# Optimization experiments

Measured on AMD Instinct MI355X. Metric: run time of the kernel, lower is better.

Reference implementation:

```python
import jax, jax.numpy as jnp
import numpy as np

B, N, DIM, IN_DIM, H = 8, 3136, 147, 64, 1
HD = IN_DIM // H          # per-head value/key dim = 64
MLP_HID = int(IN_DIM * 1.0)
EPS = 1e-5


def _ln(x, w, b):
    m = jnp.mean(x, axis=-1, keepdims=True)
    v = jnp.mean((x - m) ** 2, axis=-1, keepdims=True)
    return (x - m) / jnp.sqrt(v + EPS) * w + b


def setup_inputs() -> dict:
    key = jax.random.key(0)
    ks = jax.random.split(key, 12)
    r = lambda k, shp, s=0.02: (jax.random.normal(k, shp, dtype=jnp.float32) * s)
    return {
        "x": jax.random.normal(ks[0], (B, N, DIM), dtype=jnp.float32),
        "norm1_w": jnp.ones((DIM,), jnp.float32),
        "norm1_b": jnp.zeros((DIM,), jnp.float32),
        "qkv_w": r(ks[1], (3 * IN_DIM, DIM)),
        "scale": jnp.full((H,), (DIM // H) ** -0.5, dtype=jnp.float32),
        "proj_w": r(ks[2], (IN_DIM, IN_DIM)),
        "proj_b": jnp.zeros((IN_DIM,), jnp.float32),
        "norm2_w": jnp.ones((IN_DIM,), jnp.float32),
        "norm2_b": jnp.zeros((IN_DIM,), jnp.float32),
        "fc1_w": r(ks[3], (MLP_HID, IN_DIM)),
        "fc1_b": jnp.zeros((MLP_HID,), jnp.float32),
        "fc2_w": r(ks[4], (IN_DIM, MLP_HID)),
        "fc2_b": jnp.zeros((IN_DIM,), jnp.float32),
    }


def reference(x, norm1_w, norm1_b, qkv_w, scale, proj_w, proj_b,
              norm2_w, norm2_b, fc1_w, fc1_b, fc2_w, fc2_b):
    h = _ln(x, norm1_w, norm1_b)                               # [B,N,DIM]
    qkv = jnp.einsum('bnc,oc->bno', h, qkv_w)                  # [B,N,3*IN_DIM]
    qkv = qkv.reshape(B, N, 3, H, HD).transpose(2, 0, 3, 1, 4)  # [3,B,H,N,HD]
    q, k, v = qkv[0], qkv[1], qkv[2]
    # LMSA: learnable per-head scale + diagonal (self) exclusion mask
    attn = jnp.einsum('bhid,bhjd->bhij', q, k) * scale[None, :, None, None]
    eye = jnp.eye(N, dtype=bool)
    attn = jnp.where(eye[None, None], -jnp.inf, attn)
    attn = jax.nn.softmax(attn, axis=-1)
    o = jnp.einsum('bhij,bhjd->bhid', attn, v)                 # [B,H,N,HD]
    o = o.transpose(0, 2, 1, 3).reshape(B, N, IN_DIM)
    o = jnp.einsum('bnd,od->bno', o, proj_w) + proj_b
    # num_heads == 1 -> residual is v itself
    x_attn = v[:, 0] + o                                       # [B,N,IN_DIM]
    h2 = _ln(x_attn, norm2_w, norm2_b)
    h2 = jax.nn.gelu(jnp.einsum('bnd,hd->bnh', h2, fc1_w) + fc1_b,
                     approximate=False)
    h2 = jnp.einsum('bnh,oh->bno', h2, fc2_w) + fc2_b
    return x_attn + h2
```

## Files before the change

### kernel.cpp

```cpp
#include <hip/hip_runtime.h>
#include <math.h>
#include <stdint.h>

#define B_    8
#define N_    3136
#define DIM_  147
#define KP_   160
#define TOK_  (B_*N_)
#define QKV3_ 192
#define NSPLIT 4

typedef __attribute__((ext_vector_type(4)))  float f32x4;
typedef __attribute__((ext_vector_type(16))) float f32x16;
typedef __attribute__((ext_vector_type(4)))  unsigned int u32x4;
typedef __attribute__((ext_vector_type(2)))  unsigned int u32x2;
typedef __attribute__((ext_vector_type(8)))  short short8;
typedef float f32x4u __attribute__((ext_vector_type(4), aligned(4)));
typedef union { short8 s; u32x4 u; } pk8;

static __device__ __forceinline__ unsigned short f2b(float f){
  unsigned int u = __float_as_uint(f);
  u += 0x7fffu + ((u>>16)&1u);
  return (unsigned short)(u>>16);
}
static __device__ __forceinline__ unsigned int pk2(float a, float b){
  return ((unsigned int)f2b(b)<<16) | (unsigned int)f2b(a);
}
static __device__ __forceinline__ unsigned int pk2t(float a, float b){
  return (__float_as_uint(b) & 0xffff0000u) | (__float_as_uint(a)>>16);
}
static __device__ __forceinline__ float b2f(unsigned short s){
  return __uint_as_float(((unsigned int)s)<<16);
}

#define GLD16(gp, lp) __builtin_amdgcn_global_load_lds( \
    reinterpret_cast<const uint32_t __attribute__((address_space(1)))*>(reinterpret_cast<uintptr_t>(gp)), \
    reinterpret_cast<uint32_t __attribute__((address_space(3)))*>(reinterpret_cast<uintptr_t>(lp)), \
    16, 0, 0)

__global__ __launch_bounds__(256) void k_qkv(const float* __restrict__ x,
                                             const float* __restrict__ w1,
                                             const float* __restrict__ b1,
                                             const float* __restrict__ qkvw,
                                             const float* __restrict__ scale,
                                             unsigned short* __restrict__ qb,
                                             unsigned short* __restrict__ kb,
                                             unsigned short* __restrict__ vtb,
                                             unsigned short* __restrict__ vfb){
  __shared__ alignas(16) unsigned short Wb[192*168];
  unsigned short* A_ = Wb;
  unsigned short* VT = Wb;
  int tid = threadIdx.x;
  int w = tid>>6, lane = tid&63, quad = lane>>4, l16 = lane&15;
  int t0 = blockIdx.x*64;
  float sc2 = scale[0] * 1.44269504089f;

  #pragma unroll
  for(int half=0; half<2; half++){
    int g = half*32 + (tid>>3), e = tid&7;
    const float* xr = x + (size_t)(t0+g)*147;
    f32x4u xv[5];
    float s = 0.f, sq = 0.f;
    #pragma unroll
    for(int j=0;j<5;j++){
      int k = e + 8*j;
      int keff = (k > 36) ? 36 : k;
      f32x4u v = *(const f32x4u*)(xr + 4*keff);
      if(j == 4){
        v[0] = (k<=36) ? v[0] : 0.f;
        v[1] = (k<=36) ? v[1] : 0.f;
        v[2] = (k<=36) ? v[2] : 0.f;
        v[3] = (k< 36) ? v[3] : 0.f;
      }
      xv[j] = v;
      s  += (v[0]+v[1]) + (v[2]+v[3]);
      sq += (v[0]*v[0]+v[1]*v[1]) + (v[2]*v[2]+v[3]*v[3]);
    }
    s  += __shfl_xor(s,1,64);  s  += __shfl_xor(s,2,64);  s  += __shfl_xor(s,4,64);
    sq += __shfl_xor(sq,1,64); sq += __shfl_xor(sq,2,64); sq += __shfl_xor(sq,4,64);
    float mean = s*(1.f/147.f);
    float var  = sq*(1.f/147.f) - mean*mean;
    float rstd = rsqrtf(var + 1e-5f);
    #pragma unroll
    for(int j=0;j<5;j++){
      int k = e + 8*j;
      unsigned int lo = 0u, hi = 0u;
      if(k <= 36){
        int c0 = 4*k;
        int c3 = (k==36) ? 146 : c0+3;
        float y0 = (xv[j][0]-mean)*rstd*w1[c0]   + b1[c0];
        float y1 = (xv[j][1]-mean)*rstd*w1[c0+1] + b1[c0+1];
        float y2 = (xv[j][2]-mean)*rstd*w1[c0+2] + b1[c0+2];
        float y3 = (xv[j][3]-mean)*rstd*w1[c3]   + b1[c3];
        if(k == 36) y3 = 0.f;
        lo = pk2(y0,y1); hi = pk2(y2,y3);
      }
      *(u32x2*)(A_ + g*168 + 4*k) = (u32x2){lo,hi};
    }
  }
  __syncthreads();
  short8 Af[5];
  #pragma unroll
  for(int kk=0;kk<5;kk++)
    Af[kk] = *(const short8*)(A_ + (w*16+l16)*168 + kk*32 + quad*8);
  __syncthreads();
  {
    unsigned int* dst = (unsigned int*)Wb;
    #pragma unroll
    for(int rep=0; rep<15; rep++){
      int idx = rep*256 + tid;
      int row = idx/20, c = idx - row*20;
      u32x4 o = (u32x4){0u,0u,0u,0u};
      if(c < 19){
        const float* sp = qkvw + row*147 + c*8;
        f32x4u a = *(const f32x4u*)sp;
        o[0] = pk2(a[0],a[1]);
        if(c < 18){
          f32x4u bv = *(const f32x4u*)(sp+4);
          o[1] = pk2(a[2],a[3]);
          o[2] = pk2(bv[0],bv[1]);
          o[3] = pk2(bv[2],bv[3]);
        } else {
          o[1] = pk2(a[2],0.f);
        }
      }
      *(u32x4*)(dst + row*84 + c*4) = o;
    }
  }
  __syncthreads();
  f32x4 acc[12];
  #pragma unroll
  for(int i=0;i<12;i++) acc[i] = (f32x4){0.f,0.f,0.f,0.f};
  #pragma unroll
  for(int nt=0;nt<12;nt++){
    #pragma unroll
    for(int kk=0;kk<5;kk++){
      short8 Bf = *(const short8*)(Wb + (nt*16+l16)*168 + kk*32 + quad*8);
      acc[nt] = __builtin_amdgcn_mfma_f32_16x16x32_bf16(Af[kk], Bf, acc[nt], 0,0,0);
    }
  }
  #pragma unroll
  for(int nt=0;nt<12;nt++){
    int o = nt*16 + l16;
    #pragma unroll
    for(int r=0;r<4;r++){
      int tl = w*16 + quad*4 + r;
      int mg = t0 + tl;
      float val = acc[nt][r];
      if(o < 64)        qb[(size_t)mg*64 + o]        = f2b(val*sc2);
      else if(o < 128)  kb[(size_t)mg*64 + (o-64)]   = f2b(val);
      else              vfb[(size_t)mg*64 + (o-128)] = f2b(val);
    }
  }
  __syncthreads();
  #pragma unroll
  for(int nt=8;nt<12;nt++){
    int hd = (nt-8)*16 + l16;
    #pragma unroll
    for(int r=0;r<4;r++)
      VT[hd*72 + (w*16 + quad*4 + r)] = f2b(acc[nt][r]);
  }
  __syncthreads();
  {
    int b = t0 / N_, n0 = t0 - b*N_;
    const unsigned int* VT32 = (const unsigned int*)VT;
    unsigned int* vg = (unsigned int*)vtb + ((size_t)b*64)*(N_/2) + (n0>>1);
    #pragma unroll
    for(int rep=0;rep<8;rep++){
      int f = rep*256 + tid;
      int row = f>>5, c = f&31;
      vg[(size_t)row*(N_/2) + c] = VT32[row*36 + c];
    }
  }
}

__global__ __launch_bounds__(128,2) void k_attn(const unsigned short* __restrict__ qb,
                                                const unsigned short* __restrict__ kb,
                                                const unsigned short* __restrict__ vtb,
                                                unsigned short* __restrict__ Opart,
                                                float* __restrict__ lpart){
  __shared__ alignas(16) unsigned int L[8192];
  __shared__ float Lr[128];
  int tid = threadIdx.x;
  int w = tid>>6, lane = tid&63;
  int h = lane>>5, l32 = lane&31, l7 = l32&7;
  int qt = blockIdx.x, sp = blockIdx.y, b = blockIdx.z;
  int q0 = qt*64;
  int kv0 = (sp*49)>>2, kv1 = ((sp+1)*49)>>2;
  int nt = kv1 - kv0;

  short8 Qf[2][4];
  {
    const unsigned short* qg = qb + ((size_t)b*N_ + q0)*64;
    #pragma unroll
    for(int qh=0;qh<2;qh++)
      #pragma unroll
      for(int kc=0;kc<4;kc++)
        Qf[qh][kc] = *(const short8*)(qg + (32*qh + l32)*64 + 16*kc + 8*h);
  }
  int koffG[4], voffG[4];
  {
    int pl = lane>>3, cl = lane&7;
    #pragma unroll
    for(int rr=0;rr<4;rr++){
      int p = rr*8 + pl;
      int sig = (p & 0x13) | ((p&4)<<1) | ((p&8)>>1);
      int cx = cl ^ (p&7);
      koffG[rr] = (32*w + sig)*128 + cx*16;
      voffG[rr] = (32*w + p)*(N_*2) + cx*16;
    }
  }
  const char* kBase = (const char*)kb + (size_t)b*N_*128;
  const char* vBase = (const char*)vtb + (size_t)b*64*(size_t)(N_*2);

  f32x16 O[2][2];
  #pragma unroll
  for(int qh=0;qh<2;qh++) for(int hdq=0;hdq<2;hdq++)
    #pragma unroll
    for(int r=0;r<16;r++) O[qh][hdq][r] = 0.f;
  float lracc[2][4];
  #pragma unroll
  for(int qh=0;qh<2;qh++)
    #pragma unroll
    for(int j=0;j<4;j++) lracc[qh][j] = 0.f;

  {
    const char* kT = kBase + (size_t)kv0*8192;
    const char* vT = vBase + (size_t)kv0*128;
    #pragma unroll
    for(int rr=0;rr<4;rr++) GLD16(kT + koffG[rr], (char*)L + w*4096 + rr*1024);
    #pragma unroll
    for(int rr=0;rr<4;rr++) GLD16(vT + voffG[rr], (char*)L + 8192 + w*4096 + rr*1024);
  }

  int cur = 0;
  for(int i=0;i<nt;i++){
    int kvt = kv0 + i;
    if(i+1 < nt){
      const char* kT = kBase + (size_t)(kvt+1)*8192;
      const char* vT = vBase + (size_t)(kvt+1)*128;
      char* dst = (char*)L + (cur^1)*16384;
      #pragma unroll
      for(int rr=0;rr<4;rr++) GLD16(kT + koffG[rr], dst + w*4096 + rr*1024);
      #pragma unroll
      for(int rr=0;rr<4;rr++) GLD16(vT + voffG[rr], dst + 8192 + w*4096 + rr*1024);
      asm volatile("s_waitcnt vmcnt(8)" ::: "memory");
    } else {
      asm volatile("s_waitcnt vmcnt(0)" ::: "memory");
    }
    __builtin_amdgcn_s_barrier();
    __builtin_amdgcn_sched_barrier(0);

    const unsigned short* Kh = (const unsigned short*)L + cur*8192 + w*2048;
    const unsigned short* Vh = (const unsigned short*)L + cur*8192 + 4096;

    short8 Kf[4];
    #pragma unroll
    for(int kc=0;kc<4;kc++)
      Kf[kc] = *(const short8*)(Kh + l32*64 + (((2*kc+h) ^ l7)&7)*8);
    #pragma unroll
    for(int qh=0;qh<2;qh++){
      f32x16 S;
      #pragma unroll
      for(int r=0;r<16;r++) S[r] = 0.f;
      #pragma unroll
      for(int kc=0;kc<4;kc++)
        S = __builtin_amdgcn_mfma_f32_32x32x16_bf16(Kf[kc], Qf[qh][kc], S, 0,0,0);
      f32x16 E;
      if(kvt == qt){
        int dref = 32*qh + l32 - 32*w - 8*h;
        #pragma unroll
        for(int r=0;r<16;r++){
          int kvl = 16*((r>>3)&1) + 4*((r>>2)&1) + (r&3);
          float pv = (kvl == dref) ? 0.f : __builtin_amdgcn_exp2f(S[r]);
          E[r] = pv; lracc[qh][r&3] += pv;
        }
      } else {
        #pragma unroll
        for(int r=0;r<16;r++){
          float pv = __builtin_amdgcn_exp2f(S[r]);
          E[r] = pv; lracc[qh][r&3] += pv;
        }
      }
      pk8 Pb0, Pb1;
      Pb0.u = (u32x4){ pk2t(E[0],E[1]),   pk2t(E[2],E[3]),
                       pk2t(E[4],E[5]),   pk2t(E[6],E[7]) };
      Pb1.u = (u32x4){ pk2t(E[8],E[9]),   pk2t(E[10],E[11]),
                       pk2t(E[12],E[13]), pk2t(E[14],E[15]) };
      #pragma unroll
      for(int hdq=0;hdq<2;hdq++){
        short8 Vf0 = *(const short8*)(Vh + (32*hdq + l32)*64 + (((4*w + h) ^ l7)&7)*8);
        short8 Vf1 = *(const short8*)(Vh + (32*hdq + l32)*64 + (((4*w + 2 + h) ^ l7)&7)*8);
        O[qh][hdq] = __builtin_amdgcn_mfma_f32_32x32x16_bf16(Vf0, Pb0.s, O[qh][hdq], 0,0,0);
        O[qh][hdq] = __builtin_amdgcn_mfma_f32_32x32x16_bf16(Vf1, Pb1.s, O[qh][hdq], 0,0,0);
      }
    }
    __builtin_amdgcn_sched_barrier(0);
    asm volatile("" ::: "memory");
    __builtin_amdgcn_s_barrier();
    cur ^= 1;
  }
  float lr[2];
  #pragma unroll
  for(int qh=0;qh<2;qh++)
    lr[qh] = (lracc[qh][0] + lracc[qh][1]) + (lracc[qh][2] + lracc[qh][3]);
  lr[0] += __shfl_xor(lr[0],32,64);
  lr[1] += __shfl_xor(lr[1],32,64);
  __syncthreads();
  if(w == 0){
    #pragma unroll
    for(int qh=0;qh<2;qh++)
      #pragma unroll
      for(int hdq=0;hdq<2;hdq++)
        #pragma unroll
        for(int r=0;r<16;r++)
          L[(qh*32 + hdq*16 + r)*64 + lane] = __float_as_uint(O[qh][hdq][r]);
    Lr[lane]      = lr[0];
    Lr[64 + lane] = lr[1];
  }
  __syncthreads();
  if(w == 1){
    #pragma unroll
    for(int qh=0;qh<2;qh++)
      #pragma unroll
      for(int hdq=0;hdq<2;hdq++)
        #pragma unroll
        for(int r=0;r<16;r++)
          O[qh][hdq][r] += __uint_as_float(L[(qh*32 + hdq*16 + r)*64 + lane]);
    float lt0 = lr[0] + Lr[lane];
    float lt1 = lr[1] + Lr[64 + lane];
    size_t lb = (size_t)sp*TOK_ + (size_t)b*N_ + q0;
    if(lane < 32){ lpart[lb + lane] = lt0; lpart[lb + 32 + lane] = lt1; }
    #pragma unroll
    for(int qh=0;qh<2;qh++){
      int q = 32*qh + l32;
      #pragma unroll
      for(int hdq=0;hdq<2;hdq++)
        #pragma unroll
        for(int k2=0;k2<8;k2++){
          int idx = 16*hdq + 4*(k2>>1) + 2*h + (k2&1);
          L[q*36 + idx] = pk2(O[qh][hdq][2*k2], O[qh][hdq][2*k2+1]);
        }
    }
    unsigned int* og = (unsigned int*)(Opart + ((size_t)sp*TOK_ + (size_t)b*N_ + q0)*64);
    #pragma unroll
    for(int rep=0;rep<8;rep++){
      int f = rep*64 + lane;
      int row = f>>3, c4 = f&7;
      *(u32x4*)(og + row*32 + c4*4) = *(const u32x4*)&L[row*36 + c4*4];
    }
  }
}

__global__ __launch_bounds__(256) void k_mlp(const unsigned short* __restrict__ Opart,
                                             const float* __restrict__ lpart,
                                             const unsigned short* __restrict__ vfb,
                                             const float* __restrict__ projw,
                                             const float* __restrict__ fc1w,
                                             const float* __restrict__ fc2w,
                                             const float* __restrict__ projb,
                                             const float* __restrict__ n2w,
                                             const float* __restrict__ n2b,
                                             const float* __restrict__ fc1b,
                                             const float* __restrict__ fc2b,
                                             float* __restrict__ out){
  __shared__ alignas(16) unsigned short Ws[3][64*72];
  __shared__ alignas(16) unsigned short Xs[64*72];
  unsigned int* Xs32 = (unsigned int*)Xs;
  int tid = threadIdx.x;
  int w = tid>>6, lane = tid&63, quad = lane>>4, l16 = lane&15;
  int t0 = blockIdx.x*64;

  {
    #pragma unroll
    for(int rep=0;rep<2;rep++){
      int f = rep*256 + tid;
      int row = f>>3, c = f&7;
      int so = (row<<6) + (c<<3);
      f32x4 a0 = *(const f32x4*)(projw + so), b0 = *(const f32x4*)(projw + so + 4);
      f32x4 a1 = *(const f32x4*)(fc1w  + so), b1v = *(const f32x4*)(fc1w  + so + 4);
      f32x4 a2 = *(const f32x4*)(fc2w  + so), b2 = *(const f32x4*)(fc2w  + so + 4);
      *(u32x4*)((unsigned int*)Ws[0] + row*36 + c*4) =
        (u32x4){pk2(a0[0],a0[1]),pk2(a0[2],a0[3]),pk2(b0[0],b0[1]),pk2(b0[2],b0[3])};
      *(u32x4*)((unsigned int*)Ws[1] + row*36 + c*4) =
        (u32x4){pk2(a1[0],a1[1]),pk2(a1[2],a1[3]),pk2(b1v[0],b1v[1]),pk2(b1v[2],b1v[3])};
      *(u32x4*)((unsigned int*)Ws[2] + row*36 + c*4) =
        (u32x4){pk2(a2[0],a2[1]),pk2(a2[2],a2[3]),pk2(b2[0],b2[1]),pk2(b2[2],b2[3])};
    }
  }
  #pragma unroll
  for(int i=0;i<2;i++){
    int f = i*256 + tid;
    int row = f>>3, c = f&7;
    float lo[4] = {0,0,0,0}, hi[4] = {0,0,0,0};
    float lsum = 0.f;
    #pragma unroll
    for(int s=0;s<NSPLIT;s++){
      u32x4 a = *((const u32x4*)(Opart + ((size_t)s*TOK_ + t0)*64) + row*8 + c);
      #pragma unroll
      for(int k=0;k<4;k++){
        lo[k] += __uint_as_float(a[k]<<16);
        hi[k] += __uint_as_float(a[k] & 0xffff0000u);
      }
      lsum += lpart[(size_t)s*TOK_ + t0 + row];
    }
    float linv = 1.f/lsum;
    u32x4 o;
    #pragma unroll
    for(int k=0;k<4;k++) o[k] = pk2(lo[k]*linv, hi[k]*linv);
    *(u32x4*)&Xs32[row*36 + c*4] = o;
  }
  __syncthreads();

  short8 Af[2];
  #pragma unroll
  for(int kk=0;kk<2;kk++)
    Af[kk] = *(const short8*)(Xs + (w*16+l16)*72 + kk*32 + quad*8);
  f32x4 acc[4];
  #pragma unroll
  for(int i=0;i<4;i++) acc[i] = (f32x4){0.f,0.f,0.f,0.f};
  #pragma unroll
  for(int jt=0;jt<4;jt++)
    #pragma unroll
    for(int kk=0;kk<2;kk++){
      short8 Bf = *(const short8*)(Ws[0] + (jt*16+l16)*72 + kk*32 + quad*8);
      acc[jt] = __builtin_amdgcn_mfma_f32_16x16x32_bf16(Af[kk], Bf, acc[jt], 0,0,0);
    }
  float xa[4][4];
  #pragma unroll
  for(int jt=0;jt<4;jt++){
    int col = jt*16 + l16;
    float pb = projb[col];
    #pragma unroll
    for(int r=0;r<4;r++){
      int tg = t0 + w*16 + quad*4 + r;
      xa[jt][r] = acc[jt][r] + pb + b2f(vfb[(size_t)tg*64 + col]);
    }
  }
  #pragma unroll
  for(int r=0;r<4;r++){
    float s = 0.f, sq = 0.f;
    #pragma unroll
    for(int jt=0;jt<4;jt++){ s += xa[jt][r]; sq += xa[jt][r]*xa[jt][r]; }
    s  += __shfl_xor(s,1,64);  s  += __shfl_xor(s,2,64);
    s  += __shfl_xor(s,4,64);  s  += __shfl_xor(s,8,64);
    sq += __shfl_xor(sq,1,64); sq += __shfl_xor(sq,2,64);
    sq += __shfl_xor(sq,4,64); sq += __shfl_xor(sq,8,64);
    float mu = s*(1.f/64.f);
    float var = sq*(1.f/64.f) - mu*mu;
    float rstd = rsqrtf(var + 1e-5f);
    #pragma unroll
    for(int jt=0;jt<4;jt++){
      int col = jt*16 + l16;
      Xs[(w*16+quad*4+r)*72 + col] = f2b((xa[jt][r]-mu)*rstd*n2w[col] + n2b[col]);
    }
  }
  #pragma unroll
  for(int kk=0;kk<2;kk++)
    Af[kk] = *(const short8*)(Xs + (w*16+l16)*72 + kk*32 + quad*8);
  f32x4 acc2[4];
  #pragma unroll
  for(int i=0;i<4;i++) acc2[i] = (f32x4){0.f,0.f,0.f,0.f};
  #pragma unroll
  for(int jt=0;jt<4;jt++)
    #pragma unroll
    for(int kk=0;kk<2;kk++){
      short8 Bf = *(const short8*)(Ws[1] + (jt*16+l16)*72 + kk*32 + quad*8);
      acc2[jt] = __builtin_amdgcn_mfma_f32_16x16x32_bf16(Af[kk], Bf, acc2[jt], 0,0,0);
    }
  #pragma unroll
  for(int jt=0;jt<4;jt++){
    int col = jt*16 + l16;
    float fb = fc1b[col];
    #pragma unroll
    for(int r=0;r<4;r++){
      float g = acc2[jt][r] + fb;
      float z = g*0.70710678118f;
      float az = fabsf(z);
      float t = 1.f/(1.f + 0.3275911f*az);
      float poly = ((((1.061405429f*t - 1.453152027f)*t + 1.421413741f)*t - 0.284496736f)*t + 0.254829592f)*t;
      float er = 1.f - poly*__builtin_amdgcn_exp2f(-az*az*1.44269504089f);
      er = (z < 0.f) ? -er : er;
      Xs[(w*16+quad*4+r)*72 + col] = f2b(0.5f*g*(1.f + er));
    }
  }
  #pragma unroll
  for(int kk=0;kk<2;kk++)
    Af[kk] = *(const short8*)(Xs + (w*16+l16)*72 + kk*32 + quad*8);
  f32x4 acc3[4];
  #pragma unroll
  for(int i=0;i<4;i++) acc3[i] = (f32x4){0.f,0.f,0.f,0.f};
  #pragma unroll
  for(int jt=0;jt<4;jt++)
    #pragma unroll
    for(int kk=0;kk<2;kk++){
      short8 Bf = *(const short8*)(Ws[2] + (jt*16+l16)*72 + kk*32 + quad*8);
      acc3[jt] = __builtin_amdgcn_mfma_f32_16x16x32_bf16(Af[kk], Bf, acc3[jt], 0,0,0);
    }
  #pragma unroll
  for(int jt=0;jt<4;jt++){
    int col = jt*16 + l16;
    float ob2 = fc2b[col];
    #pragma unroll
    for(int r=0;r<4;r++){
      int tg = t0 + w*16 + quad*4 + r;
      out[(size_t)tg*64 + col] = xa[jt][r] + acc3[jt][r] + ob2;
    }
  }
}

extern "C" void kernel_launch(void* const* d_in, const int* in_sizes, int n_in,
                              void* d_out, int out_size, void* d_ws, size_t ws_size,
                              hipStream_t stream){
  const float* x     = (const float*)d_in[0];
  const float* n1w   = (const float*)d_in[1];
  const float* n1b   = (const float*)d_in[2];
  const float* qkvw  = (const float*)d_in[3];
  const float* scale = (const float*)d_in[4];
  const float* projw = (const float*)d_in[5];
  const float* projb = (const float*)d_in[6];
  const float* n2w   = (const float*)d_in[7];
  const float* n2b   = (const float*)d_in[8];
  const float* fc1w  = (const float*)d_in[9];
  const float* fc1b  = (const float*)d_in[10];
  const float* fc2w  = (const float*)d_in[11];
  const float* fc2b  = (const float*)d_in[12];

  char* base = (char*)d_ws;
  unsigned short* qb  = (unsigned short*)(base + 0);
  unsigned short* kb  = (unsigned short*)(base + 3211264);
  unsigned short* vtb = (unsigned short*)(base + 6422528);
  unsigned short* vfb = (unsigned short*)(base + 9633792);
  unsigned short* Op  = (unsigned short*)(base + 12845056);
  float*          lp  = (float*)(base + 25690112);

  hipLaunchKernelGGL(k_qkv,  dim3(TOK_/64),    dim3(256), 0, stream,
                     x, n1w, n1b, qkvw, scale, qb, kb, vtb, vfb);
  hipLaunchKernelGGL(k_attn, dim3(49,NSPLIT,8), dim3(128), 0, stream, qb, kb, vtb, Op, lp);
  hipLaunchKernelGGL(k_mlp,  dim3(TOK_/64),    dim3(256), 0, stream, Op, lp, vfb,
                     projw, fc1w, fc2w, projb, n2w, n2b, fc1b, fc2b, (float*)d_out);
}
```

Measured before the change: 144.8 us.

## Share K/V LDS tiles across two query tiles per attention block

Each attention block now has 256 threads covering two 64-row query tiles. The four waves split the K/V tile loads between them (two waves load K, two load V), so each staged KV tile in shared memory serves twice as many queries. The aim is to halve the global-to-LDS traffic per query and cut the per-wave load instructions. The trade-off is a padding query tile in the last block (49 tiles is odd), which does no compute but still joins the barriers, plus a larger block that may change occupancy.

```diff
diff --git a/kernel.cpp b/kernel.cpp
--- a/kernel.cpp
+++ b/kernel.cpp
@@ -174,18 +174,23 @@
   }
 }
 
-__global__ __launch_bounds__(128,2) void k_attn(const unsigned short* __restrict__ qb,
+__global__ __launch_bounds__(256,4) void k_attn(const unsigned short* __restrict__ qb,
                                                 const unsigned short* __restrict__ kb,
                                                 const unsigned short* __restrict__ vtb,
                                                 unsigned short* __restrict__ Opart,
                                                 float* __restrict__ lpart){
   __shared__ alignas(16) unsigned int L[8192];
-  __shared__ float Lr[128];
+  __shared__ float Lr[256];
   int tid = threadIdx.x;
-  int w = tid>>6, lane = tid&63;
+  int s = tid>>6;
+  int w2 = s>>1;
+  int w  = s&1;
+  int lane = tid&63;
   int h = lane>>5, l32 = lane&31, l7 = l32&7;
   int qt = blockIdx.x, sp = blockIdx.y, b = blockIdx.z;
-  int q0 = qt*64;
+  int qtile = 2*qt + w2;
+  int live = (qtile < 49);
+  int q0 = live ? qtile*64 : 0;
   int kv0 = (sp*49)>>2, kv1 = ((sp+1)*49)>>2;
   int nt = kv1 - kv0;
 
@@ -198,20 +203,27 @@
       for(int kc=0;kc<4;kc++)
         Qf[qh][kc] = *(const short8*)(qg + (32*qh + l32)*64 + 16*kc + 8*h);
   }
-  int koffG[4], voffG[4];
+  int isK = (s < 2);
+  int wh  = s & 1;
+  int offG[4];
   {
     int pl = lane>>3, cl = lane&7;
     #pragma unroll
     for(int rr=0;rr<4;rr++){
       int p = rr*8 + pl;
-      int sig = (p & 0x13) | ((p&4)<<1) | ((p&8)>>1);
       int cx = cl ^ (p&7);
-      koffG[rr] = (32*w + sig)*128 + cx*16;
-      voffG[rr] = (32*w + p)*(N_*2) + cx*16;
-    }
-  }
-  const char* kBase = (const char*)kb + (size_t)b*N_*128;
-  const char* vBase = (const char*)vtb + (size_t)b*64*(size_t)(N_*2);
+      if(isK){
+        int sig = (p & 0x13) | ((p&4)<<1) | ((p&8)>>1);
+        offG[rr] = (32*wh + sig)*128 + cx*16;
+      } else {
+        offG[rr] = (32*wh + p)*(N_*2) + cx*16;
+      }
+    }
+  }
+  const char* sBase = isK ? ((const char*)kb  + (size_t)b*N_*128)
+                          : ((const char*)vtb + (size_t)b*64*(size_t)(N_*2));
+  int tileStride = isK ? 8192 : 128;
+  int ldsOff = (isK ? 0 : 8192) + wh*4096;
 
   f32x16 O[2][2];
   #pragma unroll
@@ -225,74 +237,70 @@
     for(int j=0;j<4;j++) lracc[qh][j] = 0.f;
 
   {
-    const char* kT = kBase + (size_t)kv0*8192;
-    const char* vT = vBase + (size_t)kv0*128;
-    #pragma unroll
-    for(int rr=0;rr<4;rr++) GLD16(kT + koffG[rr], (char*)L + w*4096 + rr*1024);
-    #pragma unroll
-    for(int rr=0;rr<4;rr++) GLD16(vT + voffG[rr], (char*)L + 8192 + w*4096 + rr*1024);
+    const char* tp = sBase + (size_t)kv0*tileStride;
+    #pragma unroll
+    for(int rr=0;rr<4;rr++) GLD16(tp + offG[rr], (char*)L + ldsOff + rr*1024);
   }
 
   int cur = 0;
   for(int i=0;i<nt;i++){
     int kvt = kv0 + i;
     if(i+1 < nt){
-      const char* kT = kBase + (size_t)(kvt+1)*8192;
-      const char* vT = vBase + (size_t)(kvt+1)*128;
-      char* dst = (char*)L + (cur^1)*16384;
-      #pragma unroll
-      for(int rr=0;rr<4;rr++) GLD16(kT + koffG[rr], dst + w*4096 + rr*1024);
-      #pragma unroll
-      for(int rr=0;rr<4;rr++) GLD16(vT + voffG[rr], dst + 8192 + w*4096 + rr*1024);
-      asm volatile("s_waitcnt vmcnt(8)" ::: "memory");
+      const char* tp = sBase + (size_t)(kvt+1)*tileStride;
+      char* dst = (char*)L + (cur^1)*16384 + ldsOff;
+      #pragma unroll
+      for(int rr=0;rr<4;rr++) GLD16(tp + offG[rr], dst + rr*1024);
+      asm volatile("s_waitcnt vmcnt(4)" ::: "memory");
     } else {
       asm volatile("s_waitcnt vmcnt(0)" ::: "memory");
     }
     __builtin_amdgcn_s_barrier();
     __builtin_amdgcn_sched_barrier(0);
 
-    const unsigned short* Kh = (const unsigned short*)L + cur*8192 + w*2048;
-    const unsigned short* Vh = (const unsigned short*)L + cur*8192 + 4096;
-
-    short8 Kf[4];
-    #pragma unroll
-    for(int kc=0;kc<4;kc++)
-      Kf[kc] = *(const short8*)(Kh + l32*64 + (((2*kc+h) ^ l7)&7)*8);
-    #pragma unroll
-    for(int qh=0;qh<2;qh++){
-      f32x16 S;
-      #pragma unroll
-      for(int r=0;r<16;r++) S[r] = 0.f;
+    if(live){
+      const unsigned short* Kh = (const unsigned short*)L + cur*8192 + w*2048;
+      const unsigned short* Vh = (const unsigned short*)L + cur*8192 + 4096;
+
+      short8 Kf[4];
       #pragma unroll
       for(int kc=0;kc<4;kc++)
-        S = __builtin_amdgcn_mfma_f32_32x32x16_bf16(Kf[kc], Qf[qh][kc], S, 0,0,0);
-      f32x16 E;
-      if(kvt == qt){
-        int dref = 32*qh + l32 - 32*w - 8*h;
+        Kf[kc] = *(const short8*)(Kh + l32*64 + (((2*kc+h) ^ l7)&7)*8);
+      #pragma unroll
+      for(int qh=0;qh<2;qh++){
+        f32x16 S;
         #pragma unroll
-        for(int r=0;r<16;r++){
-          int kvl = 16*((r>>3)&1) + 4*((r>>2)&1) + (r&3);
-          float pv = (kvl == dref) ? 0.f : __builtin_amdgcn_exp2f(S[r]);
-          E[r] = pv; lracc[qh][r&3] += pv;
+        for(int r=0;r<16;r++) S[r] = 0.f;
+        #pragma unroll
+        for(int kc=0;kc<4;kc++)
+          S = __builtin_amdgcn_mfma_f32_32x32x16_bf16(Kf[kc], Qf[qh][kc], S, 0,0,0);
+        f32x16 E;
+        if(kvt == qtile){
+          int dref = 32*qh + l32 - 32*w - 8*h;
+          #pragma unroll
+          for(int r=0;r<16;r++){
+            int kvl = 16*((r>>3)&1) + 4*((r>>2)&1) + (r&3);
+            float pv = (kvl == dref) ? 0.f : __builtin_amdgcn_exp2f(S[r]);
+            E[r] = pv; lracc[qh][r&3] += pv;
+          }
+        } else {
+          #pragma unroll
+          for(int r=0;r<16;r++){
+            float pv = __builtin_amdgcn_exp2f(S[r]);
+            E[r] = pv; lracc[qh][r&3] += pv;
+          }
         }
-      } else {
+        pk8 Pb0, Pb1;
+        Pb0.u = (u32x4){ pk2t(E[0],E[1]),   pk2t(E[2],E[3]),
+                         pk2t(E[4],E[5]),   pk2t(E[6],E[7]) };
+        Pb1.u = (u32x4){ pk2t(E[8],E[9]),   pk2t(E[10],E[11]),
+                         pk2t(E[12],E[13]), pk2t(E[14],E[15]) };
         #pragma unroll
-        for(int r=0;r<16;r++){
-          float pv = __builtin_amdgcn_exp2f(S[r]);
-          E[r] = pv; lracc[qh][r&3] += pv;
+        for(int hdq=0;hdq<2;hdq++){
+          short8 Vf0 = *(const short8*)(Vh + (32*hdq + l32)*64 + (((4*w + h) ^ l7)&7)*8);
+          short8 Vf1 = *(const short8*)(Vh + (32*hdq + l32)*64 + (((4*w + 2 + h) ^ l7)&7)*8);
+          O[qh][hdq] = __builtin_amdgcn_mfma_f32_32x32x16_bf16(Vf0, Pb0.s, O[qh][hdq], 0,0,0);
+          O[qh][hdq] = __builtin_amdgcn_mfma_f32_32x32x16_bf16(Vf1, Pb1.s, O[qh][hdq], 0,0,0);
         }
-      }
-      pk8 Pb0, Pb1;
-      Pb0.u = (u32x4){ pk2t(E[0],E[1]),   pk2t(E[2],E[3]),
-                       pk2t(E[4],E[5]),   pk2t(E[6],E[7]) };
-      Pb1.u = (u32x4){ pk2t(E[8],E[9]),   pk2t(E[10],E[11]),
-                       pk2t(E[12],E[13]), pk2t(E[14],E[15]) };
-      #pragma unroll
-      for(int hdq=0;hdq<2;hdq++){
-        short8 Vf0 = *(const short8*)(Vh + (32*hdq + l32)*64 + (((4*w + h) ^ l7)&7)*8);
-        short8 Vf1 = *(const short8*)(Vh + (32*hdq + l32)*64 + (((4*w + 2 + h) ^ l7)&7)*8);
-        O[qh][hdq] = __builtin_amdgcn_mfma_f32_32x32x16_bf16(Vf0, Pb0.s, O[qh][hdq], 0,0,0);
-        O[qh][hdq] = __builtin_amdgcn_mfma_f32_32x32x16_bf16(Vf1, Pb1.s, O[qh][hdq], 0,0,0);
       }
     }
     __builtin_amdgcn_sched_barrier(0);
@@ -307,6 +315,8 @@
   lr[0] += __shfl_xor(lr[0],32,64);
   lr[1] += __shfl_xor(lr[1],32,64);
   __syncthreads();
+  unsigned int* Lp = L + w2*4096;
+  float* Lrp = Lr + w2*128;
   if(w == 0){
     #pragma unroll
     for(int qh=0;qh<2;qh++)
@@ -314,9 +324,9 @@
       for(int hdq=0;hdq<2;hdq++)
         #pragma unroll
         for(int r=0;r<16;r++)
-          L[(qh*32 + hdq*16 + r)*64 + lane] = __float_as_uint(O[qh][hdq][r]);
-    Lr[lane]      = lr[0];
-    Lr[64 + lane] = lr[1];
+          Lp[(qh*32 + hdq*16 + r)*64 + lane] = __float_as_uint(O[qh][hdq][r]);
+    Lrp[lane]      = lr[0];
+    Lrp[64 + lane] = lr[1];
   }
   __syncthreads();
   if(w == 1){
@@ -326,11 +336,11 @@
       for(int hdq=0;hdq<2;hdq++)
         #pragma unroll
         for(int r=0;r<16;r++)
-          O[qh][hdq][r] += __uint_as_float(L[(qh*32 + hdq*16 + r)*64 + lane]);
-    float lt0 = lr[0] + Lr[lane];
-    float lt1 = lr[1] + Lr[64 + lane];
+          O[qh][hdq][r] += __uint_as_float(Lp[(qh*32 + hdq*16 + r)*64 + lane]);
+    float lt0 = lr[0] + Lrp[lane];
+    float lt1 = lr[1] + Lrp[64 + lane];
     size_t lb = (size_t)sp*TOK_ + (size_t)b*N_ + q0;
-    if(lane < 32){ lpart[lb + lane] = lt0; lpart[lb + 32 + lane] = lt1; }
+    if(live && lane < 32){ lpart[lb + lane] = lt0; lpart[lb + 32 + lane] = lt1; }
     #pragma unroll
     for(int qh=0;qh<2;qh++){
       int q = 32*qh + l32;
@@ -339,15 +349,17 @@
         #pragma unroll
         for(int k2=0;k2<8;k2++){
           int idx = 16*hdq + 4*(k2>>1) + 2*h + (k2&1);
-          L[q*36 + idx] = pk2(O[qh][hdq][2*k2], O[qh][hdq][2*k2+1]);
+          Lp[q*36 + idx] = pk2(O[qh][hdq][2*k2], O[qh][hdq][2*k2+1]);
         }
     }
-    unsigned int* og = (unsigned int*)(Opart + ((size_t)sp*TOK_ + (size_t)b*N_ + q0)*64);
-    #pragma unroll
-    for(int rep=0;rep<8;rep++){
-      int f = rep*64 + lane;
-      int row = f>>3, c4 = f&7;
-      *(u32x4*)(og + row*32 + c4*4) = *(const u32x4*)&L[row*36 + c4*4];
+    if(live){
+      unsigned int* og = (unsigned int*)(Opart + ((size_t)sp*TOK_ + (size_t)b*N_ + q0)*64);
+      #pragma unroll
+      for(int rep=0;rep<8;rep++){
+        int f = rep*64 + lane;
+        int row = f>>3, c4 = f&7;
+        *(u32x4*)(og + row*32 + c4*4) = *(const u32x4*)&Lp[row*36 + c4*4];
+      }
     }
   }
 }
@@ -536,7 +548,7 @@
 
   hipLaunchKernelGGL(k_qkv,  dim3(TOK_/64),    dim3(256), 0, stream,
                      x, n1w, n1b, qkvw, scale, qb, kb, vtb, vfb);
-  hipLaunchKernelGGL(k_attn, dim3(49,NSPLIT,8), dim3(128), 0, stream, qb, kb, vtb, Op, lp);
+  hipLaunchKernelGGL(k_attn, dim3(25,NSPLIT,8), dim3(256), 0, stream, qb, kb, vtb, Op, lp);
   hipLaunchKernelGGL(k_mlp,  dim3(TOK_/64),    dim3(256), 0, stream, Op, lp, vfb,
                      projw, fc1w, fc2w, projb, n2w, n2b, fc1b, fc2b, (float*)d_out);
 }
```

New measurement: 264.8 us. 1.83x slower.

## Load K/V fragments directly into registers, drop LDS double buffering in attention

Applied to the files above, without the earlier changes.

Replaces the LDS-staged, double-buffered K/V tile pipeline (global_load_lds plus block barriers) with per-wave direct global-to-register loads of the K and V MFMA fragments, prefetched two tiles ahead in register sets K0/K1 and V0/V1. This removes the LDS round trip and the per-tile s_barrier synchronisation, and shrinks the LDS array. In exchange it uses more VGPRs, which may pressure the two-blocks-per-SIMD launch bound. Each wave now issues its own global loads, so data previously shared through LDS is fetched once per wave through the caches.

```diff
diff --git a/kernel.cpp b/kernel.cpp
--- a/kernel.cpp
+++ b/kernel.cpp
@@ -32,11 +32,6 @@
 static __device__ __forceinline__ float b2f(unsigned short s){
   return __uint_as_float(((unsigned int)s)<<16);
 }
-
-#define GLD16(gp, lp) __builtin_amdgcn_global_load_lds( \
-    reinterpret_cast<const uint32_t __attribute__((address_space(1)))*>(reinterpret_cast<uintptr_t>(gp)), \
-    reinterpret_cast<uint32_t __attribute__((address_space(3)))*>(reinterpret_cast<uintptr_t>(lp)), \
-    16, 0, 0)
 
 __global__ __launch_bounds__(256) void k_qkv(const float* __restrict__ x,
                                              const float* __restrict__ w1,
@@ -179,11 +174,11 @@
                                                 const unsigned short* __restrict__ vtb,
                                                 unsigned short* __restrict__ Opart,
                                                 float* __restrict__ lpart){
-  __shared__ alignas(16) unsigned int L[8192];
+  __shared__ alignas(16) unsigned int L[4096];
   __shared__ float Lr[128];
   int tid = threadIdx.x;
   int w = tid>>6, lane = tid&63;
-  int h = lane>>5, l32 = lane&31, l7 = l32&7;
+  int h = lane>>5, l32 = lane&31;
   int qt = blockIdx.x, sp = blockIdx.y, b = blockIdx.z;
   int q0 = qt*64;
   int kv0 = (sp*49)>>2, kv1 = ((sp+1)*49)>>2;
@@ -198,20 +193,19 @@
       for(int kc=0;kc<4;kc++)
         Qf[qh][kc] = *(const short8*)(qg + (32*qh + l32)*64 + 16*kc + 8*h);
   }
-  int koffG[4], voffG[4];
-  {
-    int pl = lane>>3, cl = lane&7;
-    #pragma unroll
-    for(int rr=0;rr<4;rr++){
-      int p = rr*8 + pl;
-      int sig = (p & 0x13) | ((p&4)<<1) | ((p&8)>>1);
-      int cx = cl ^ (p&7);
-      koffG[rr] = (32*w + sig)*128 + cx*16;
-      voffG[rr] = (32*w + p)*(N_*2) + cx*16;
-    }
-  }
-  const char* kBase = (const char*)kb + (size_t)b*N_*128;
-  const char* vBase = (const char*)vtb + (size_t)b*64*(size_t)(N_*2);
+  int sig32 = (l32 & 0x13) | ((l32&4)<<1) | ((l32&8)>>1);
+  const unsigned short* kR = kb + ((size_t)b*N_ + (size_t)kv0*64 + 32*w + sig32)*64 + 8*h;
+  const unsigned short* vR0 = vtb + (size_t)b*64*N_ + (size_t)l32*N_ + (size_t)kv0*64 + (4*w+h)*8;
+  const unsigned short* vR1 = vR0 + (size_t)32*N_;
+
+  short8 K0[4], K1[4], V0[4], V1[4];
+#define LDK(DST, T) { const unsigned short* p_ = kR + (size_t)(T)*4096; \
+    DST[0]=*(const short8*)(p_);    DST[1]=*(const short8*)(p_+16); \
+    DST[2]=*(const short8*)(p_+32); DST[3]=*(const short8*)(p_+48); }
+#define LDV(DST, T) { const unsigned short* p0_ = vR0 + (size_t)(T)*64; \
+    const unsigned short* p1_ = vR1 + (size_t)(T)*64; \
+    DST[0]=*(const short8*)(p0_); DST[1]=*(const short8*)(p0_+16); \
+    DST[2]=*(const short8*)(p1_); DST[3]=*(const short8*)(p1_+16); }
 
   f32x16 O[2][2];
   #pragma unroll
@@ -224,82 +218,61 @@
     #pragma unroll
     for(int j=0;j<4;j++) lracc[qh][j] = 0.f;
 
-  {
-    const char* kT = kBase + (size_t)kv0*8192;
-    const char* vT = vBase + (size_t)kv0*128;
-    #pragma unroll
-    for(int rr=0;rr<4;rr++) GLD16(kT + koffG[rr], (char*)L + w*4096 + rr*1024);
-    #pragma unroll
-    for(int rr=0;rr<4;rr++) GLD16(vT + voffG[rr], (char*)L + 8192 + w*4096 + rr*1024);
-  }
-
-  int cur = 0;
-  for(int i=0;i<nt;i++){
-    int kvt = kv0 + i;
-    if(i+1 < nt){
-      const char* kT = kBase + (size_t)(kvt+1)*8192;
-      const char* vT = vBase + (size_t)(kvt+1)*128;
-      char* dst = (char*)L + (cur^1)*16384;
-      #pragma unroll
-      for(int rr=0;rr<4;rr++) GLD16(kT + koffG[rr], dst + w*4096 + rr*1024);
-      #pragma unroll
-      for(int rr=0;rr<4;rr++) GLD16(vT + voffG[rr], dst + 8192 + w*4096 + rr*1024);
-      asm volatile("s_waitcnt vmcnt(8)" ::: "memory");
-    } else {
-      asm volatile("s_waitcnt vmcnt(0)" ::: "memory");
-    }
-    __builtin_amdgcn_s_barrier();
-    __builtin_amdgcn_sched_barrier(0);
-
-    const unsigned short* Kh = (const unsigned short*)L + cur*8192 + w*2048;
-    const unsigned short* Vh = (const unsigned short*)L + cur*8192 + 4096;
-
-    short8 Kf[4];
-    #pragma unroll
-    for(int kc=0;kc<4;kc++)
-      Kf[kc] = *(const short8*)(Kh + l32*64 + (((2*kc+h) ^ l7)&7)*8);
-    #pragma unroll
-    for(int qh=0;qh<2;qh++){
-      f32x16 S;
-      #pragma unroll
-      for(int r=0;r<16;r++) S[r] = 0.f;
-      #pragma unroll
-      for(int kc=0;kc<4;kc++)
-        S = __builtin_amdgcn_mfma_f32_32x32x16_bf16(Kf[kc], Qf[qh][kc], S, 0,0,0);
-      f32x16 E;
-      if(kvt == qt){
-        int dref = 32*qh + l32 - 32*w - 8*h;
-        #pragma unroll
-        for(int r=0;r<16;r++){
-          int kvl = 16*((r>>3)&1) + 4*((r>>2)&1) + (r&3);
-          float pv = (kvl == dref) ? 0.f : __builtin_amdgcn_exp2f(S[r]);
-          E[r] = pv; lracc[qh][r&3] += pv;
-        }
-      } else {
-        #pragma unroll
-        for(int r=0;r<16;r++){
-          float pv = __builtin_amdgcn_exp2f(S[r]);
-          E[r] = pv; lracc[qh][r&3] += pv;
-        }
-      }
-      pk8 Pb0, Pb1;
-      Pb0.u = (u32x4){ pk2t(E[0],E[1]),   pk2t(E[2],E[3]),
-                       pk2t(E[4],E[5]),   pk2t(E[6],E[7]) };
-      Pb1.u = (u32x4){ pk2t(E[8],E[9]),   pk2t(E[10],E[11]),
-                       pk2t(E[12],E[13]), pk2t(E[14],E[15]) };
-      #pragma unroll
-      for(int hdq=0;hdq<2;hdq++){
-        short8 Vf0 = *(const short8*)(Vh + (32*hdq + l32)*64 + (((4*w + h) ^ l7)&7)*8);
-        short8 Vf1 = *(const short8*)(Vh + (32*hdq + l32)*64 + (((4*w + 2 + h) ^ l7)&7)*8);
-        O[qh][hdq] = __builtin_amdgcn_mfma_f32_32x32x16_bf16(Vf0, Pb0.s, O[qh][hdq], 0,0,0);
-        O[qh][hdq] = __builtin_amdgcn_mfma_f32_32x32x16_bf16(Vf1, Pb1.s, O[qh][hdq], 0,0,0);
-      }
-    }
-    __builtin_amdgcn_sched_barrier(0);
-    asm volatile("" ::: "memory");
-    __builtin_amdgcn_s_barrier();
-    cur ^= 1;
-  }
+  LDK(K0,0); LDV(V0,0);
+  LDK(K1,1); LDV(V1,1);
+
+  int i = 0;
+#define TILESTEP(KC,VC) { \
+    int kvt = kv0 + i; \
+    _Pragma("unroll") \
+    for(int qh=0;qh<2;qh++){ \
+      f32x16 S; \
+      _Pragma("unroll") \
+      for(int r=0;r<16;r++) S[r] = 0.f; \
+      _Pragma("unroll") \
+      for(int kc=0;kc<4;kc++) \
+        S = __builtin_amdgcn_mfma_f32_32x32x16_bf16(KC[kc], Qf[qh][kc], S, 0,0,0); \
+      f32x16 E; \
+      if(kvt == qt){ \
+        int dref = 32*qh + l32 - 32*w - 8*h; \
+        _Pragma("unroll") \
+        for(int r=0;r<16;r++){ \
+          int kvl = 16*((r>>3)&1) + 4*((r>>2)&1) + (r&3); \
+          float pv = (kvl == dref) ? 0.f : __builtin_amdgcn_exp2f(S[r]); \
+          E[r] = pv; lracc[qh][r&3] += pv; \
+        } \
+      } else { \
+        _Pragma("unroll") \
+        for(int r=0;r<16;r++){ \
+          float pv = __builtin_amdgcn_exp2f(S[r]); \
+          E[r] = pv; lracc[qh][r&3] += pv; \
+        } \
+      } \
+      pk8 Pb0, Pb1; \
+      Pb0.u = (u32x4){ pk2t(E[0],E[1]),   pk2t(E[2],E[3]), \
+                       pk2t(E[4],E[5]),   pk2t(E[6],E[7]) }; \
+      Pb1.u = (u32x4){ pk2t(E[8],E[9]),   pk2t(E[10],E[11]), \
+                       pk2t(E[12],E[13]), pk2t(E[14],E[15]) }; \
+      O[qh][0] = __builtin_amdgcn_mfma_f32_32x32x16_bf16(VC[0], Pb0.s, O[qh][0], 0,0,0); \
+      O[qh][0] = __builtin_amdgcn_mfma_f32_32x32x16_bf16(VC[1], Pb1.s, O[qh][0], 0,0,0); \
+      O[qh][1] = __builtin_amdgcn_mfma_f32_32x32x16_bf16(VC[2], Pb0.s, O[qh][1], 0,0,0); \
+      O[qh][1] = __builtin_amdgcn_mfma_f32_32x32x16_bf16(VC[3], Pb1.s, O[qh][1], 0,0,0); \
+    } \
+    { int pf_ = i + 2; if(pf_ > nt-1) pf_ = nt-1;    \
+      LDK(KC, pf_); LDV(VC, pf_); } \
+    __builtin_amdgcn_sched_barrier(0); \
+    i++; }
+
+  while(i + 2 <= nt){
+    TILESTEP(K0,V0);
+    TILESTEP(K1,V1);
+  }
+  if(i < nt){ TILESTEP(K0,V0); }
+
+#undef TILESTEP
+#undef LDK
+#undef LDV
+
   float lr[2];
   #pragma unroll
   for(int qh=0;qh<2;qh++)
```

Result: slower. 161.1 us (+11.3%).

## Give each wave a private K/V staging buffer and drop per-tile block barriers

Applied to the files above, without the earlier changes.

Each of the two waves now loads its own K slice and a full copy of the V tile into a private double-buffered LDS region, so no wave reads data written by the other. This lets the two s_barrier calls per KV tile be removed, so the waves no longer stall on each other. In exchange, V traffic from global memory doubles per block and LDS use rises from 32 KB to 48 KB, which may reduce how many blocks fit per CU. The wait count is raised to match the larger number of in-flight loads.

```diff
diff --git a/kernel.cpp b/kernel.cpp
--- a/kernel.cpp
+++ b/kernel.cpp
@@ -179,7 +179,7 @@
                                                 const unsigned short* __restrict__ vtb,
                                                 unsigned short* __restrict__ Opart,
                                                 float* __restrict__ lpart){
-  __shared__ alignas(16) unsigned int L[8192];
+  __shared__ alignas(16) char LB[49152];
   __shared__ float Lr[128];
   int tid = threadIdx.x;
   int w = tid>>6, lane = tid&63;
@@ -198,20 +198,33 @@
       for(int kc=0;kc<4;kc++)
         Qf[qh][kc] = *(const short8*)(qg + (32*qh + l32)*64 + 16*kc + 8*h);
   }
-  int koffG[4], voffG[4];
+  int koffG[4], voffG[8];
   {
     int pl = lane>>3, cl = lane&7;
     #pragma unroll
     for(int rr=0;rr<4;rr++){
       int p = rr*8 + pl;
       int sig = (p & 0x13) | ((p&4)<<1) | ((p&8)>>1);
-      int cx = cl ^ (p&7);
-      koffG[rr] = (32*w + sig)*128 + cx*16;
-      voffG[rr] = (32*w + p)*(N_*2) + cx*16;
+      koffG[rr] = (32*w + sig)*128 + (cl ^ (p&7))*16;
+    }
+    #pragma unroll
+    for(int rr=0;rr<8;rr++){
+      int p = rr*8 + pl;
+      voffG[rr] = p*(N_*2) + (cl ^ (p&7))*16;
     }
   }
   const char* kBase = (const char*)kb + (size_t)b*N_*128;
   const char* vBase = (const char*)vtb + (size_t)b*64*(size_t)(N_*2);
+  char* wbuf0 = LB + w*12288;
+  char* wbuf1 = LB + 24576 + w*12288;
+
+#define STAGE(bufp, T) { \
+    const char* kT_ = kBase + (size_t)(T)*8192; \
+    const char* vT_ = vBase + (size_t)(T)*128; \
+    _Pragma("unroll") \
+    for(int rr=0;rr<4;rr++) GLD16(kT_ + koffG[rr], (bufp) + rr*1024); \
+    _Pragma("unroll") \
+    for(int rr=0;rr<8;rr++) GLD16(vT_ + voffG[rr], (bufp) + 4096 + rr*1024); }
 
   f32x16 O[2][2];
   #pragma unroll
@@ -224,35 +237,22 @@
     #pragma unroll
     for(int j=0;j<4;j++) lracc[qh][j] = 0.f;
 
-  {
-    const char* kT = kBase + (size_t)kv0*8192;
-    const char* vT = vBase + (size_t)kv0*128;
-    #pragma unroll
-    for(int rr=0;rr<4;rr++) GLD16(kT + koffG[rr], (char*)L + w*4096 + rr*1024);
-    #pragma unroll
-    for(int rr=0;rr<4;rr++) GLD16(vT + voffG[rr], (char*)L + 8192 + w*4096 + rr*1024);
-  }
-
-  int cur = 0;
+  STAGE(wbuf0, kv0);
+
   for(int i=0;i<nt;i++){
     int kvt = kv0 + i;
+    char* cb = (i&1) ? wbuf1 : wbuf0;
+    char* nb = (i&1) ? wbuf0 : wbuf1;
     if(i+1 < nt){
-      const char* kT = kBase + (size_t)(kvt+1)*8192;
-      const char* vT = vBase + (size_t)(kvt+1)*128;
-      char* dst = (char*)L + (cur^1)*16384;
-      #pragma unroll
-      for(int rr=0;rr<4;rr++) GLD16(kT + koffG[rr], dst + w*4096 + rr*1024);
-      #pragma unroll
-      for(int rr=0;rr<4;rr++) GLD16(vT + voffG[rr], dst + 8192 + w*4096 + rr*1024);
-      asm volatile("s_waitcnt vmcnt(8)" ::: "memory");
+      STAGE(nb, kvt+1);
+      asm volatile("s_waitcnt vmcnt(12)" ::: "memory");
     } else {
       asm volatile("s_waitcnt vmcnt(0)" ::: "memory");
     }
-    __builtin_amdgcn_s_barrier();
     __builtin_amdgcn_sched_barrier(0);
 
-    const unsigned short* Kh = (const unsigned short*)L + cur*8192 + w*2048;
-    const unsigned short* Vh = (const unsigned short*)L + cur*8192 + 4096;
+    const unsigned short* Kh = (const unsigned short*)cb;
+    const unsigned short* Vh = (const unsigned short*)(cb + 4096);
 
     short8 Kf[4];
     #pragma unroll
@@ -296,16 +296,16 @@
       }
     }
     __builtin_amdgcn_sched_barrier(0);
-    asm volatile("" ::: "memory");
-    __builtin_amdgcn_s_barrier();
-    cur ^= 1;
-  }
+  }
+#undef STAGE
+
   float lr[2];
   #pragma unroll
   for(int qh=0;qh<2;qh++)
     lr[qh] = (lracc[qh][0] + lracc[qh][1]) + (lracc[qh][2] + lracc[qh][3]);
   lr[0] += __shfl_xor(lr[0],32,64);
   lr[1] += __shfl_xor(lr[1],32,64);
+  unsigned int* L = (unsigned int*)LB;
   __syncthreads();
   if(w == 0){
     #pragma unroll
```

After: 153.0 us. 5.7% more time.
